# Optimization experiments

Hardware: AMD Instinct MI355X
Metric: run time of the kernel (lower is better)

## Reference

```python
import jax, jax.numpy as jnp
from jax import lax
import numpy as np


def setup_inputs() -> dict:
    key = jax.random.key(0)
    B, N, K_ORDERS = 8, 16384, 4
    k1, k2 = jax.random.split(key)
    coord = jax.random.normal(k1, (B * N, 3), dtype=jnp.float32)
    serialized_code = jax.random.randint(k2, (K_ORDERS, B * N), 0, 1 << 30)
    return {
        "coord": coord,
        "serialized_code": serialized_code,
        "batch_size": 8,
        "num_group": 1024,
        "group_size": 32,
    }


def _fps(pts, G):
    """Farthest point sampling on pts [N,3]; starts at index 0 (pointops convention)."""
    N = pts.shape[0]

    def step(carry, _):
        dist, last = carry
        d = jnp.sum((pts - pts[last]) ** 2, axis=-1)  # [N]
        dist = jnp.minimum(dist, d)
        nxt = jnp.argmax(dist).astype(jnp.int32)
        return (dist, nxt), nxt

    init = (jnp.full((N,), jnp.inf, pts.dtype), jnp.int32(0))
    _, rest = lax.scan(step, init, None, length=G - 1)
    return jnp.concatenate([jnp.zeros((1,), jnp.int32), rest])  # [G]


def reference(coord, serialized_code, batch_size, num_group, group_size):
    B, G, S = batch_size, num_group, group_size
    N = coord.shape[0] // B
    pts = coord.reshape(B, N, 3)

    # --- FPS per cloud (offset-batched in the original) ---
    loc_idx = jax.vmap(lambda p: _fps(p, G))(pts)  # [B, G] local indices
    s_idx = (loc_idx + (jnp.arange(B, dtype=jnp.int32) * N)[:, None]).reshape(-1)  # [B*G] global
    s_xyz = coord[s_idx]  # [B*G, 3]

    # --- KNN per cloud: S nearest points to each sampled center ---
    centers = s_xyz.reshape(B, G, 3)

    def knn_one(p, c):  # p [N,3], c [G,3]
        # squared distances via gemm to avoid [G,N,3] intermediate
        d2 = (jnp.sum(c * c, -1)[:, None] + jnp.sum(p * p, -1)[None, :]
              - 2.0 * c @ p.T)  # [G, N]
        _, idx = lax.top_k(-d2, S)  # ascending distance, self first
        return idx

    nloc = jax.vmap(knn_one)(pts, centers)  # [B, G, S]
    s_n_idx = (nloc + (jnp.arange(B) * N)[:, None, None]).reshape(B * G, S)

    # relative coords, drop the self point (column 0)
    s_n = coord[s_n_idx] - s_xyz[:, None, :]  # [B*G, S, 3]
    s_n = s_n[:, 1:, :]  # [B*G, S-1, 3]

    # --- serialization order over sampled points + inverse permutation ---
    code_sel = serialized_code[:, s_idx]  # [K, B*G]
    s_order = jnp.argsort(code_sel, axis=1)  # [K, B*G]
    M = s_order.shape[1]
    src = jnp.broadcast_to(jnp.arange(M, dtype=s_order.dtype), s_order.shape)
    rows = jnp.arange(s_order.shape[0])[:, None]
    s_inverse = jnp.zeros_like(s_order).at[rows, s_order].set(src)

    return s_idx, s_n, s_xyz, s_order, s_inverse
```

## Files before the change

### kernel.cpp

```cpp
#include <hip/hip_runtime.h>
#include <hip/hip_bf16.h>
#include <stdint.h>

#define BB 8
#define NN 16384
#define GG 1024
#define SS 32
#define BN (BB*NN)

#define OFF_SIDX 0
#define OFF_SN   8192
#define OFF_SXYZ 770048
#define OFF_ORD  794624
#define OFF_INV  827392

#define WS_SIDX 0
#define WS_KNN  32768

typedef float v2f __attribute__((ext_vector_type(2)));

static __device__ __forceinline__ v2f vmin2(v2f a, v2f b) {
    v2f r; r.x = fminf(a.x, b.x); r.y = fminf(a.y, b.y); return r;
}
static __device__ __forceinline__ v2f vmax2(v2f a, v2f b) {
    v2f r; r.x = fmaxf(a.x, b.x); r.y = fmaxf(a.y, b.y); return r;
}

template<int CTRL, int RM, int BM>
static __device__ __forceinline__ unsigned dpp_umax(unsigned v) {
    unsigned o = (unsigned)__builtin_amdgcn_update_dpp((int)v, (int)v, CTRL, RM, BM, false);
    return o > v ? o : v;
}

template<int CTRL, int RM, int BM>
static __device__ __forceinline__ uint64_t dpp_umin64(uint64_t v) {
    unsigned lo = (unsigned)v, hi = (unsigned)(v >> 32);
    unsigned olo = (unsigned)__builtin_amdgcn_update_dpp((int)lo, (int)lo, CTRL, RM, BM, false);
    unsigned ohi = (unsigned)__builtin_amdgcn_update_dpp((int)hi, (int)hi, CTRL, RM, BM, false);
    uint64_t o = ((uint64_t)ohi << 32) | olo;
    return o < v ? o : v;
}

static __device__ __forceinline__ uint64_t wave_umin64(uint64_t v) {
    v = dpp_umin64<0x111, 0xf, 0xf>(v);
    v = dpp_umin64<0x112, 0xf, 0xf>(v);
    v = dpp_umin64<0x114, 0xf, 0xf>(v);
    v = dpp_umin64<0x118, 0xf, 0xf>(v);
    v = dpp_umin64<0x142, 0xa, 0xf>(v);
    v = dpp_umin64<0x143, 0xc, 0xf>(v);
    return v;
}

static __device__ __forceinline__ uint64_t rdlane64(uint64_t v, int sl) {
    unsigned lo = (unsigned)__builtin_amdgcn_readlane((int)(unsigned)v, sl);
    unsigned hi = (unsigned)__builtin_amdgcn_readlane((int)(unsigned)(v >> 32), sl);
    return ((uint64_t)hi << 32) | lo;
}

static __device__ __forceinline__ unsigned mono(float f) {
    unsigned u = __float_as_uint(f);
    return u ^ (unsigned)((((int)u) >> 31) | (int)0x80000000u);
}

__global__ __launch_bounds__(1024)
__attribute__((amdgpu_waves_per_eu(4, 4)))
void fps_kernel(const float* __restrict__ coord,
                int* __restrict__ ws_sidx,
                float* __restrict__ out) {
#pragma clang fp contract(off)
    const int b = blockIdx.x;
    const int t = threadIdx.x;
    const int base = b * NN;
    const int wave = t >> 6, lane = t & 63;

    const float q0x = coord[3*base], q0y = coord[3*base+1], q0z = coord[3*base+2];

    v2f px[8], py[8], pz[8], dist[8];
#pragma unroll
    for (int j = 0; j < 8; j++) {
        int pA = t + (j << 11);
        int pB = pA + 1024;
        px[j] = (v2f){coord[3*(base+pA)  ], coord[3*(base+pB)  ]};
        py[j] = (v2f){coord[3*(base+pA)+1], coord[3*(base+pB)+1]};
        pz[j] = (v2f){coord[3*(base+pA)+2], coord[3*(base+pB)+2]};
        v2f dx = px[j] - (v2f){q0x,q0x};
        v2f dy = py[j] - (v2f){q0y,q0y};
        v2f dz = pz[j] - (v2f){q0z,q0z};
        dist[j] = (dx*dx + dy*dy) + dz*dz;
    }

    __shared__ unsigned wv[16];
    __shared__ unsigned win[2];

    if (t == 0) {
        ws_sidx[b*GG] = base;
        out[OFF_SIDX + b*GG] = (float)base;
        win[0] = 0xffffffffu; win[1] = 0xffffffffu;
    }
    __syncthreads();

    for (int g = 1; g < GG; g++) {
        const int s = g & 1;
        v2f m01 = vmax2(dist[0], dist[1]);
        v2f m23 = vmax2(dist[2], dist[3]);
        v2f m45 = vmax2(dist[4], dist[5]);
        v2f m67 = vmax2(dist[6], dist[7]);
        v2f m07 = vmax2(vmax2(m01, m23), vmax2(m45, m67));
        float bvf = fmaxf(m07.x, m07.y);
        unsigned lb = __float_as_uint(bvf);
        unsigned r = lb;
        r = dpp_umax<0x111, 0xf, 0xf>(r);
        r = dpp_umax<0x112, 0xf, 0xf>(r);
        r = dpp_umax<0x114, 0xf, 0xf>(r);
        r = dpp_umax<0x118, 0xf, 0xf>(r);
        r = dpp_umax<0x142, 0xa, 0xf>(r);
        r = dpp_umax<0x143, 0xc, 0xf>(r);
        unsigned wmax = (unsigned)__builtin_amdgcn_readlane((int)r, 63);
        if (lane == 0) wv[wave] = wmax;
        __syncthreads();
        if (t == 0) win[1 - s] = 0xffffffffu;
        unsigned x = wv[lane & 15];
        x = dpp_umax<0x111, 0xf, 0xf>(x);
        x = dpp_umax<0x112, 0xf, 0xf>(x);
        x = dpp_umax<0x114, 0xf, 0xf>(x);
        x = dpp_umax<0x118, 0xf, 0xf>(x);
        unsigned bmax = (unsigned)__builtin_amdgcn_readlane((int)x, 15);
        if (lb == bmax) {
            int e = 15;
#pragma unroll
            for (int jj = 15; jj >= 0; jj--) {
                float v = (jj & 1) ? dist[jj >> 1].y : dist[jj >> 1].x;
                if (__float_as_uint(v) == bmax) e = jj;
            }
            atomicMin(&win[s], (unsigned)(t + (e << 10)));
        }
        __syncthreads();
        unsigned pw = win[s];
        int sp = __builtin_amdgcn_readfirstlane((int)pw);
        if (t == 0) {
            ws_sidx[b*GG + g] = base + sp;
            out[OFF_SIDX + b*GG + g] = (float)(base + sp);
        }
        float qx = coord[3*(base+sp)];
        float qy = coord[3*(base+sp)+1];
        float qz = coord[3*(base+sp)+2];
        v2f qvx = (v2f){qx,qx}, qvy = (v2f){qy,qy}, qvz = (v2f){qz,qz};
#pragma unroll
        for (int j = 0; j < 8; j++) {
            v2f dx = px[j] - qvx, dy = py[j] - qvy, dz = pz[j] - qvz;
            v2f d  = (dx*dx + dy*dy) + dz*dz;
            dist[j] = vmin2(dist[j], d);
        }
    }
}

__global__ __launch_bounds__(64) void knn_kernel(const float* __restrict__ coord,
                                                 const int* __restrict__ ws_sidx,
                                                 int* __restrict__ ws_knn) {
#pragma clang fp contract(off)
    const int c = blockIdx.x;
    const int l = threadIdx.x;
    const int b = c >> 10;
    const int base = b * NN;
    const int sg = ws_sidx[c];
    const float cx = coord[3*sg], cy = coord[3*sg+1], cz = coord[3*sg+2];
    const float cc = (cx*cx + cy*cy) + cz*cz;

    uint64_t k1 = ~0ull, k2 = ~0ull;
#pragma unroll 4
    for (int j = 0; j < 256; j++) {
        int p = l + (j << 6);
        float x = coord[3*(base+p)], y = coord[3*(base+p)+1], z = coord[3*(base+p)+2];
        float pp  = (x*x + y*y) + z*z;
        float dot = (cx*x + cy*y) + cz*z;
        float d2  = (cc + pp) - 2.0f*dot;
        uint64_t key = (((uint64_t)mono(d2)) << 14) | (unsigned)p;
        if (key < k1)      { k2 = k1; k1 = key; }
        else if (key < k2) { k2 = key; }
    }

    uint64_t m0 = 0, m1 = 0, m2 = 0, m3 = 0;
    uint64_t cur = k1, nxt = k2;
    bool have_nxt = true;
    int res_p = 0;
    for (int k = 0; k < SS; k++) {
        uint64_t wmin = wave_umin64(cur);
        uint64_t bkey = rdlane64(wmin, 63);
        const int bp = (int)(bkey & 16383u);
        const int w  = bp & 63;
        const int e  = bp >> 6;
        if (l == k) res_p = bp;
        bool need_rescan = false;
        if (l == w) {
            uint64_t bit = 1ull << (e & 63);
            int word = e >> 6;
            if      (word == 0) m0 |= bit;
            else if (word == 1) m1 |= bit;
            else if (word == 2) m2 |= bit;
            else                m3 |= bit;
            if (have_nxt) { cur = nxt; have_nxt = false; }
            else need_rescan = true;
        }
        if (__ballot(need_rescan)) {
            uint64_t w0 = rdlane64(m0, w), w1 = rdlane64(m1, w),
                     w2 = rdlane64(m2, w), w3 = rdlane64(m3, w);
            uint64_t best = ~0ull;
#pragma unroll
            for (int m = 0; m < 4; m++) {
                int e2 = l + (m << 6);
                uint64_t mw = (m == 0) ? w0 : ((m == 1) ? w1 : ((m == 2) ? w2 : w3));
                int p2 = w + (e2 << 6);
                float x = coord[3*(base+p2)], y = coord[3*(base+p2)+1], z = coord[3*(base+p2)+2];
                float pp  = (x*x + y*y) + z*z;
                float dot = (cx*x + cy*y) + cz*z;
                float d2  = (cc + pp) - 2.0f*dot;
                uint64_t key = (((uint64_t)mono(d2)) << 14) | (unsigned)p2;
                bool cons = (mw >> l) & 1ull;
                if (!cons && key < best) best = key;
            }
            best = wave_umin64(best);
            uint64_t rk = rdlane64(best, 63);
            if (l == w) cur = rk;
        }
    }
    if (l < SS) ws_knn[c * SS + l] = res_p;
}

__global__ void sxyz_kernel(const float* __restrict__ coord,
                            const int* __restrict__ ws_sidx,
                            float* __restrict__ out) {
    int t = blockIdx.x * blockDim.x + threadIdx.x;
    if (t < 8192*3) {
        int i = t / 3, cmp = t - 3*i;
        out[OFF_SXYZ + t] = coord[3*ws_sidx[i] + cmp];
    }
}

__global__ void sn_kernel(const float* __restrict__ coord,
                          const int* __restrict__ ws_sidx,
                          const int* __restrict__ ws_knn,
                          float* __restrict__ out) {
#pragma clang fp contract(off)
    int t = blockIdx.x * blockDim.x + threadIdx.x;
    if (t < 8192*31*3) {
        int cmp = t % 3; int rem = t / 3;
        int j = rem % 31; int i = rem / 31;
        int b = i >> 10;
        int nb = ws_knn[i*SS + j + 1];
        int gidx = b*NN + nb;
        float v = coord[3*gidx + cmp] - coord[3*ws_sidx[i] + cmp];
        out[OFF_SN + t] = v;
    }
}

__global__ __launch_bounds__(1024) void sort_kernel(const int* __restrict__ ser,
                                                    const int* __restrict__ ws_sidx,
                                                    float* __restrict__ out) {
    __shared__ uint64_t keys[8192];
    const int r = blockIdx.x, t = threadIdx.x;
#pragma unroll
    for (int s = 0; s < 8; s++) {
        int i = t + (s << 10);
        uint32_t code = (uint32_t)ser[r * BN + ws_sidx[i]];
        keys[i] = ((uint64_t)code << 13) | (uint32_t)i;
    }
    __syncthreads();
    for (int k2 = 2; k2 <= 8192; k2 <<= 1) {
        for (int j = k2 >> 1; j > 0; j >>= 1) {
#pragma unroll 2
            for (int s = 0; s < 8; s++) {
                int i = t + (s << 10);
                int ixj = i ^ j;
                if (ixj > i) {
                    uint64_t a = keys[i], bq = keys[ixj];
                    bool up = ((i & k2) == 0);
                    if ((a > bq) == up) { keys[i] = bq; keys[ixj] = a; }
                }
            }
            __syncthreads();
        }
    }
    for (int s = 0; s < 8; s++) {
        int k = t + (s << 10);
        uint64_t key = keys[k];
        int i = (int)(key & 8191u);
        out[OFF_ORD + r*8192 + k] = (float)i;
        out[OFF_INV + r*8192 + i] = (float)k;
    }
}

extern "C" void kernel_launch(void* const* d_in, const int* in_sizes, int n_in,
                              void* d_out, int out_size, void* d_ws, size_t ws_size,
                              hipStream_t stream) {
    const float* coord = (const float*)d_in[0];
    const int*   ser   = (const int*)d_in[1];
    float* out = (float*)d_out;
    char* ws = (char*)d_ws;
    int* ws_sidx = (int*)(ws + WS_SIDX);
    int* ws_knn  = (int*)(ws + WS_KNN);

    hipLaunchKernelGGL(fps_kernel,  dim3(BB),   dim3(1024), 0, stream, coord, ws_sidx, out);
    hipLaunchKernelGGL(knn_kernel,  dim3(8192), dim3(64),   0, stream, coord, ws_sidx, ws_knn);
    hipLaunchKernelGGL(sxyz_kernel, dim3(96),   dim3(256),  0, stream, coord, ws_sidx, out);
    hipLaunchKernelGGL(sn_kernel,   dim3(2976), dim3(256),  0, stream, coord, ws_sidx, ws_knn, out);
    hipLaunchKernelGGL(sort_kernel, dim3(4),    dim3(1024), 0, stream, ser, ws_sidx, out);
}
```

Before: 1.826 ms.

## Split FPS per cloud across eight cooperative blocks with global slot exchange

The farthest-point-sampling kernel now splits each cloud's 16384 points over eight workgroups of 1024 threads instead of one, so each thread keeps two points in registers instead of sixteen. Each iteration, every block publishes its local max distance and index to a global slot tagged with the iteration number. One wave per block spins on the eight slots and picks the global argmax. The kernel is launched cooperatively so all 64 blocks are co-resident, trading per-thread compute for a cross-block global-memory handshake on every one of the 1023 serial iterations.

```diff
diff --git a/kernel.cpp b/kernel.cpp
--- a/kernel.cpp
+++ b/kernel.cpp
@@ -7,6 +7,8 @@
 #define GG 1024
 #define SS 32
 #define BN (BB*NN)
+#define CHUNK 2048
+#define NBLK 8
 
 #define OFF_SIDX 0
 #define OFF_SN   8192
@@ -16,15 +18,7 @@
 
 #define WS_SIDX 0
 #define WS_KNN  32768
-
-typedef float v2f __attribute__((ext_vector_type(2)));
-
-static __device__ __forceinline__ v2f vmin2(v2f a, v2f b) {
-    v2f r; r.x = fminf(a.x, b.x); r.y = fminf(a.y, b.y); return r;
-}
-static __device__ __forceinline__ v2f vmax2(v2f a, v2f b) {
-    v2f r; r.x = fmaxf(a.x, b.x); r.y = fmaxf(a.y, b.y); return r;
-}
+#define WS_SLOT 1081344
 
 template<int CTRL, int RM, int BM>
 static __device__ __forceinline__ unsigned dpp_umax(unsigned v) {
@@ -63,51 +57,52 @@
 }
 
 __global__ __launch_bounds__(1024)
-__attribute__((amdgpu_waves_per_eu(4, 4)))
 void fps_kernel(const float* __restrict__ coord,
                 int* __restrict__ ws_sidx,
+                unsigned long long* __restrict__ slots,
                 float* __restrict__ out) {
 #pragma clang fp contract(off)
-    const int b = blockIdx.x;
+    const int blk = blockIdx.x;
+    const int b = blk >> 3;
+    const int c = blk & 7;
     const int t = threadIdx.x;
     const int base = b * NN;
+    const int cbase = c * CHUNK;
     const int wave = t >> 6, lane = t & 63;
 
     const float q0x = coord[3*base], q0y = coord[3*base+1], q0z = coord[3*base+2];
 
-    v2f px[8], py[8], pz[8], dist[8];
-#pragma unroll
-    for (int j = 0; j < 8; j++) {
-        int pA = t + (j << 11);
+    float x0,y0,z0,x1,y1,z1,d0,d1;
+    {
+        int pA = base + cbase + t;
         int pB = pA + 1024;
-        px[j] = (v2f){coord[3*(base+pA)  ], coord[3*(base+pB)  ]};
-        py[j] = (v2f){coord[3*(base+pA)+1], coord[3*(base+pB)+1]};
-        pz[j] = (v2f){coord[3*(base+pA)+2], coord[3*(base+pB)+2]};
-        v2f dx = px[j] - (v2f){q0x,q0x};
-        v2f dy = py[j] - (v2f){q0y,q0y};
-        v2f dz = pz[j] - (v2f){q0z,q0z};
-        dist[j] = (dx*dx + dy*dy) + dz*dz;
+        x0 = coord[3*pA]; y0 = coord[3*pA+1]; z0 = coord[3*pA+2];
+        x1 = coord[3*pB]; y1 = coord[3*pB+1]; z1 = coord[3*pB+2];
+        float dx = x0-q0x, dy = y0-q0y, dz = z0-q0z;
+        d0 = (dx*dx + dy*dy) + dz*dz;
+        dx = x1-q0x; dy = y1-q0y; dz = z1-q0z;
+        d1 = (dx*dx + dy*dy) + dz*dz;
     }
 
     __shared__ unsigned wv[16];
     __shared__ unsigned win[2];
+    __shared__ int      sw[2];
 
     if (t == 0) {
-        ws_sidx[b*GG] = base;
-        out[OFF_SIDX + b*GG] = (float)base;
         win[0] = 0xffffffffu; win[1] = 0xffffffffu;
+        if (c == 0) {
+            ws_sidx[b*GG] = base;
+            out[OFF_SIDX + b*GG] = (float)base;
+        }
     }
     __syncthreads();
+
+    unsigned long long* bslot = slots + b * (2*NBLK);
 
     for (int g = 1; g < GG; g++) {
         const int s = g & 1;
-        v2f m01 = vmax2(dist[0], dist[1]);
-        v2f m23 = vmax2(dist[2], dist[3]);
-        v2f m45 = vmax2(dist[4], dist[5]);
-        v2f m67 = vmax2(dist[6], dist[7]);
-        v2f m07 = vmax2(vmax2(m01, m23), vmax2(m45, m67));
-        float bvf = fmaxf(m07.x, m07.y);
-        unsigned lb = __float_as_uint(bvf);
+        unsigned bb0 = __float_as_uint(d0), bb1 = __float_as_uint(d1);
+        unsigned lb = bb0 > bb1 ? bb0 : bb1;
         unsigned r = lb;
         r = dpp_umax<0x111, 0xf, 0xf>(r);
         r = dpp_umax<0x112, 0xf, 0xf>(r);
@@ -126,31 +121,56 @@
         x = dpp_umax<0x118, 0xf, 0xf>(x);
         unsigned bmax = (unsigned)__builtin_amdgcn_readlane((int)x, 15);
         if (lb == bmax) {
-            int e = 15;
-#pragma unroll
-            for (int jj = 15; jj >= 0; jj--) {
-                float v = (jj & 1) ? dist[jj >> 1].y : dist[jj >> 1].x;
-                if (__float_as_uint(v) == bmax) e = jj;
+            int e = (bb0 == bmax) ? 0 : 1;
+            atomicMin(&win[s], (unsigned)(t + (e << 10)));
+        }
+        __syncthreads();
+        if (t == 0) {
+            unsigned pw = win[s];
+            unsigned pbatch = (unsigned)cbase + pw;
+            unsigned long long v = (((unsigned long long)bmax) << 24)
+                                 | ((unsigned long long)(unsigned)g << 14)
+                                 | pbatch;
+            __hip_atomic_store(&bslot[s*NBLK + c], v,
+                               __ATOMIC_RELEASE, __HIP_MEMORY_SCOPE_AGENT);
+        }
+        if (wave == 0) {
+            uint64_t kk = ~0ull;
+            if (lane < NBLK) {
+                const unsigned long long* sl = &bslot[s*NBLK + lane];
+                unsigned long long v;
+                do {
+                    v = __hip_atomic_load(sl, __ATOMIC_ACQUIRE,
+                                          __HIP_MEMORY_SCOPE_AGENT);
+                } while ((((unsigned)(v >> 14)) & 1023u) != (unsigned)g);
+                unsigned mb = (unsigned)(v >> 24);
+                unsigned pb = (unsigned)(v & 16383u);
+                kk = (((uint64_t)(unsigned)(~mb)) << 14) | pb;
             }
-            atomicMin(&win[s], (unsigned)(t + (e << 10)));
+            kk = dpp_umin64<0x111, 0xf, 0xf>(kk);
+            kk = dpp_umin64<0x112, 0xf, 0xf>(kk);
+            kk = dpp_umin64<0x114, 0xf, 0xf>(kk);
+            uint64_t wkey = rdlane64(kk, 7);
+            int sp = (int)(wkey & 16383u);
+            if (t == 0) {
+                sw[s] = sp;
+                if (c == 0) {
+                    ws_sidx[b*GG + g] = base + sp;
+                    out[OFF_SIDX + b*GG + g] = (float)(base + sp);
+                }
+            }
         }
         __syncthreads();
-        unsigned pw = win[s];
-        int sp = __builtin_amdgcn_readfirstlane((int)pw);
-        if (t == 0) {
-            ws_sidx[b*GG + g] = base + sp;
-            out[OFF_SIDX + b*GG + g] = (float)(base + sp);
-        }
+        int sp = sw[s];
         float qx = coord[3*(base+sp)];
         float qy = coord[3*(base+sp)+1];
         float qz = coord[3*(base+sp)+2];
-        v2f qvx = (v2f){qx,qx}, qvy = (v2f){qy,qy}, qvz = (v2f){qz,qz};
-#pragma unroll
-        for (int j = 0; j < 8; j++) {
-            v2f dx = px[j] - qvx, dy = py[j] - qvy, dz = pz[j] - qvz;
-            v2f d  = (dx*dx + dy*dy) + dz*dz;
-            dist[j] = vmin2(dist[j], d);
-        }
+        float dx = x0-qx, dy = y0-qy, dz = z0-qz;
+        float n0 = (dx*dx + dy*dy) + dz*dz;
+        dx = x1-qx; dy = y1-qy; dz = z1-qz;
+        float n1 = (dx*dx + dy*dy) + dz*dz;
+        d0 = fminf(d0, n0);
+        d1 = fminf(d1, n1);
     }
 }
 
@@ -293,13 +313,17 @@
                               void* d_out, int out_size, void* d_ws, size_t ws_size,
                               hipStream_t stream) {
     const float* coord = (const float*)d_in[0];
-    const int*   ser   = (const int*)d_in[1];
+    const int* ser = (const int*)d_in[1];
     float* out = (float*)d_out;
     char* ws = (char*)d_ws;
     int* ws_sidx = (int*)(ws + WS_SIDX);
     int* ws_knn  = (int*)(ws + WS_KNN);
-
-    hipLaunchKernelGGL(fps_kernel,  dim3(BB),   dim3(1024), 0, stream, coord, ws_sidx, out);
+    unsigned long long* slots = (unsigned long long*)(ws + WS_SLOT);
+
+    void* kargs[] = { (void*)&coord, (void*)&ws_sidx, (void*)&slots, (void*)&out };
+    hipLaunchCooperativeKernel((const void*)fps_kernel, dim3(BB*NBLK), dim3(1024),
+                               kargs, 0, stream);
+
     hipLaunchKernelGGL(knn_kernel,  dim3(8192), dim3(64),   0, stream, coord, ws_sidx, ws_knn);
     hipLaunchKernelGGL(sxyz_kernel, dim3(96),   dim3(256),  0, stream, coord, ws_sidx, out);
     hipLaunchKernelGGL(sn_kernel,   dim3(2976), dim3(256),  0, stream, coord, ws_sidx, ws_knn, out);
```

After: 2.252 ms. 23.3% more time.
